# Optimization experiments

Hardware: AMD Instinct MI355X
Metric: run time of the kernel (lower is better)

Reference implementation:

```python
import jax, jax.numpy as jnp
import numpy as np

WIN = 11
SIGMA = 1.5
C1 = 0.01 ** 2
C2 = 0.03 ** 2


def _gauss1d():
    coords = jnp.arange(WIN, dtype=jnp.float32) - WIN // 2
    g = jnp.exp(-(coords ** 2) / (2.0 * SIGMA ** 2))
    return g / g.sum()


def _blur(x, g):
    C = x.shape[1]
    pad = WIN // 2
    dn = ('NCHW', 'OIHW', 'NCHW')
    kh = jnp.tile(g.reshape(1, 1, WIN, 1), (C, 1, 1, 1))
    kw = jnp.tile(g.reshape(1, 1, 1, WIN), (C, 1, 1, 1))
    x = jax.lax.conv_general_dilated(x, kh, (1, 1), ((pad, pad), (0, 0)),
                                     dimension_numbers=dn, feature_group_count=C)
    x = jax.lax.conv_general_dilated(x, kw, (1, 1), ((0, 0), (pad, pad)),
                                     dimension_numbers=dn, feature_group_count=C)
    return x


def _ssim_loss(pred, target, loss_weight=1.0):
    g = _gauss1d()
    mu1 = _blur(pred, g)
    mu2 = _blur(target, g)
    mu1_sq = mu1 * mu1
    mu2_sq = mu2 * mu2
    mu1_mu2 = mu1 * mu2
    sigma1_sq = _blur(pred * pred, g) - mu1_sq
    sigma2_sq = _blur(target * target, g) - mu2_sq
    sigma12 = _blur(pred * target, g) - mu1_mu2
    ssim_map = ((2.0 * mu1_mu2 + C1) * (2.0 * sigma12 + C2)) / \
               ((mu1_sq + mu2_sq + C1) * (sigma1_sq + sigma2_sq + C2))
    # size_average=True -> scalar mean; reduction='mean' on a scalar is identity
    return loss_weight * (1.0 - ssim_map.mean())


def setup_inputs() -> dict:
    key = jax.random.key(0)
    k1, k2 = jax.random.split(key)
    shape = (16, 3, 512, 512)
    pred = jax.random.uniform(k1, shape, dtype=jnp.float32)
    target = jax.random.uniform(k2, shape, dtype=jnp.float32)
    return {"pred": pred, "target": target}


def reference(pred, target):
    return _ssim_loss(pred, target, loss_weight=1.0)
```

## Files before the change

### kernel.cpp

```cpp
#include <hip/hip_runtime.h>

typedef float f2 __attribute__((ext_vector_type(2)));

#define IMG 512
#define TW 32
#define TH 32
#define NG 12
#define SROW 148
#define BOFFD 96
#define N_TOT (16 * 3 * 512 * 512)
#define NBLK (256 * 48)
#define NSLOT 1024

__device__ __constant__ f2 Gw2[11] = {
    {0.00102838f, 0.00102838f}, {0.00759876f, 0.00759876f},
    {0.03600077f, 0.03600077f}, {0.10936086f, 0.10936086f},
    {0.21300537f, 0.21300537f}, {0.26601173f, 0.26601173f},
    {0.21300537f, 0.21300537f}, {0.10936086f, 0.10936086f},
    {0.03600077f, 0.03600077f}, {0.00759876f, 0.00759876f},
    {0.00102838f, 0.00102838f}};

__device__ __forceinline__ unsigned pkh(float a, float b) {
    unsigned r;
    asm("v_cvt_pkrtz_f16_f32 %0, %1, %2" : "=v"(r) : "v"(a), "v"(b));
    return r;
}
__device__ __forceinline__ f2 uph(unsigned u) {
    float lo, hi;
    const unsigned uh = u >> 16;
    asm("v_cvt_f32_f16 %0, %1" : "=v"(lo) : "v"(u));
    asm("v_cvt_f32_f16 %0, %1" : "=v"(hi) : "v"(uh));
    return (f2){lo, hi};
}

__device__ __forceinline__ void vtaps(const float4 P, const float4 T, const int k,
                                      f2 A0[4][2], f2 A1[4][2]) {
    const f2 p[2] = {{P.x, P.y}, {P.z, P.w}};
    const f2 t[2] = {{T.x, T.y}, {T.z, T.w}};
#pragma unroll
    for (int h = 0; h < 2; ++h) {
        const f2 ss = p[h] * p[h] + t[h] * t[h];
        const f2 pt = p[h] * t[h];
        if (k < 11) {
            const f2 w = Gw2[k];
            A0[0][h] += w * p[h];
            A0[1][h] += w * t[h];
            A0[2][h] += w * ss;
            A0[3][h] += w * pt;
        }
        if (k > 0) {
            const f2 w = Gw2[k - 1];
            A1[0][h] += w * p[h];
            A1[1][h] += w * t[h];
            A1[2][h] += w * ss;
            A1[3][h] += w * pt;
        }
    }
}

__global__ __launch_bounds__(256, 4) void ssim_main(const float* __restrict__ pred,
                                                    const float* __restrict__ tgt,
                                                    float* __restrict__ ws,
                                                    int parts_mode) {
    __shared__ __align__(16) float plane[TH * SROW];
    __shared__ float red[4];

    const int tid = threadIdx.x;
    const int tile = blockIdx.x;
    const int plane_id = blockIdx.y;
    const int tile_x = tile & 15;
    const int tile_y = tile >> 4;
    const int tx = tile_x * TW;
    const int ty = tile_y * TH;
    const float* pbase = pred + (size_t)plane_id * (IMG * IMG);
    const float* tbase = tgt + (size_t)plane_id * (IMG * IMG);

    if (tid < NG * 16) {
        const int g4 = tid % NG;
        const int rp = tid / NG;
        const int r0 = rp * 2;
        const int col = tx - 8 + (g4 << 2);
        const int ybase = ty + r0 - 5;

        f2 A0[4][2], A1[4][2];
#pragma unroll
        for (int q = 0; q < 4; ++q)
#pragma unroll
            for (int h = 0; h < 2; ++h) { A0[q][h] = (f2)0.f; A1[q][h] = (f2)0.f; }

        if ((unsigned)(tile_x - 1) < 14u && (unsigned)(tile_y - 1) < 14u) {
            const float* pp = pbase + (ybase * IMG + col);
            const float* tp = tbase + (ybase * IMG + col);
#pragma unroll
            for (int k = 0; k < 12; ++k) {
                const float4 P = *(const float4*)(pp + k * IMG);
                const float4 T = *(const float4*)(tp + k * IMG);
                vtaps(P, T, k, A0, A1);
            }
        } else {
            const bool xin = (unsigned)col < (unsigned)IMG;
#pragma unroll
            for (int k = 0; k < 12; ++k) {
                const int y = ybase + k;
                float4 P = make_float4(0.f, 0.f, 0.f, 0.f);
                float4 T = make_float4(0.f, 0.f, 0.f, 0.f);
                if (xin && (unsigned)y < (unsigned)IMG) {
                    const int gidx = y * IMG + col;
                    P = *(const float4*)(pbase + gidx);
                    T = *(const float4*)(tbase + gidx);
                }
                vtaps(P, T, k, A0, A1);
            }
        }

        const int cb = g4 << 2;
#pragma unroll
        for (int r = 0; r < 2; ++r) {
            f2 (*A)[2] = r ? A1 : A0;
            float* rowA = &plane[(r0 + r) * SROW + (cb << 1)];
            *(float4*)rowA       = make_float4(A[0][0].x, A[1][0].x, A[0][0].y, A[1][0].y);
            *(float4*)(rowA + 4) = make_float4(A[0][1].x, A[1][1].x, A[0][1].y, A[1][1].y);
            uint4 bv;
            bv.x = pkh(A[2][0].x, A[3][0].x);
            bv.y = pkh(A[2][0].y, A[3][0].y);
            bv.z = pkh(A[2][1].x, A[3][1].x);
            bv.w = pkh(A[2][1].y, A[3][1].y);
            *(uint4*)&plane[(r0 + r) * SROW + BOFFD + cb] = bv;
        }
    }
    __syncthreads();

    float lsum = 0.f;
    {
        const int oy = tid >> 3;
        const int ox = (tid & 7) << 2;
        const float* rowbase = &plane[oy * SROW];

        f2 acc[4];
        f2 sacc[4];
#pragma unroll
        for (int j = 0; j < 4; ++j) { acc[j] = (f2)0.f; sacc[j] = (f2)0.f; }

        {
            const float4* rowA = (const float4*)(rowbase + ((ox + 2) << 1));
#pragma unroll
            for (int i4 = 0; i4 < 8; ++i4) {
                const float4 q = rowA[i4];
                const f2 v[2] = {{q.x, q.y}, {q.z, q.w}};
#pragma unroll
                for (int h = 0; h < 2; ++h) {
                    const int i = 2 * i4 + h;
#pragma unroll
                    for (int j = 0; j < 4; ++j) {
                        const int k = i - 1 - j;
                        if (k >= 0 && k <= 10) acc[j] += Gw2[k] * v[h];
                    }
                }
            }
        }

        {
            const uint4* rowB = (const uint4*)(rowbase + BOFFD + ox);
#pragma unroll
            for (int i4 = 0; i4 < 5; ++i4) {
                const uint4 q = rowB[i4];
                const unsigned qq[4] = {q.x, q.y, q.z, q.w};
#pragma unroll
                for (int c = 0; c < 4; ++c) {
                    const int m = 4 * i4 + c;
                    if (m >= 3 && m <= 16) {
                        const f2 v = uph(qq[c]);
#pragma unroll
                        for (int j = 0; j < 4; ++j) {
                            const int k = m - 3 - j;
                            if (k >= 0 && k <= 10) sacc[j] += Gw2[k] * v;
                        }
                    }
                }
            }
        }

        const float C1 = 0.0001f;
        const float C2 = 0.0009f;
#pragma unroll
        for (int j = 0; j < 4; ++j) {
            const float m1 = acc[j].x, m2 = acc[j].y;
            const float bss = sacc[j].x, bpt = sacc[j].y;
            const float mu1s = m1 * m1;
            const float mu2s = m2 * m2;
            const float mu12 = m1 * m2;
            const float A = mu1s + mu2s;
            const float s12 = bpt - mu12;
            const float sden = bss - A;
            const float num = fmaf(2.f, mu12, C1) * fmaf(2.f, s12, C2);
            const float den = (A + C1) * (sden + C2);
            lsum += num * __builtin_amdgcn_rcpf(den);
        }
    }

#pragma unroll
    for (int off = 32; off > 0; off >>= 1) lsum += __shfl_down(lsum, off, 64);
    if ((tid & 63) == 0) red[tid >> 6] = lsum;
    __syncthreads();
    if (tid == 0) {
        const float bs = (red[0] + red[1]) + (red[2] + red[3]);
        const int bid = blockIdx.y * gridDim.x + blockIdx.x;
        if (parts_mode) {
            ws[bid] = bs;
        } else {
            atomicAdd(&ws[bid & (NSLOT - 1)], bs);
        }
    }
}

__global__ __launch_bounds__(1024) void ssim_final(const float4* __restrict__ ws4,
                                                   float* __restrict__ out, int count4) {
    __shared__ float red[16];
    const int tid = threadIdx.x;
    float s = 0.f;
    for (int i = tid; i < count4; i += 1024) {
        const float4 w = ws4[i];
        s += (w.x + w.y) + (w.z + w.w);
    }
#pragma unroll
    for (int off = 32; off > 0; off >>= 1) s += __shfl_down(s, off, 64);
    if ((tid & 63) == 0) red[tid >> 6] = s;
    __syncthreads();
    if (tid == 0) {
        float tot = 0.f;
#pragma unroll
        for (int i = 0; i < 16; ++i) tot += red[i];
        out[0] = 1.0f - tot * (1.0f / (float)N_TOT);
    }
}

extern "C" void kernel_launch(void* const* d_in, const int* in_sizes, int n_in,
                              void* d_out, int out_size, void* d_ws, size_t ws_size,
                              hipStream_t stream) {
    const float* pred = (const float*)d_in[0];
    const float* tgt = (const float*)d_in[1];
    float* out = (float*)d_out;
    float* ws = (float*)d_ws;

    const int parts_mode = (ws_size >= (size_t)NBLK * sizeof(float)) ? 1 : 0;
    if (!parts_mode) {
        hipMemsetAsync(ws, 0, NSLOT * sizeof(float), stream);
    }
    dim3 grid(256, 48);
    ssim_main<<<grid, 256, 0, stream>>>(pred, tgt, ws, parts_mode);
    ssim_final<<<1, 1024, 0, stream>>>((const float4*)ws, out,
                                       (parts_mode ? NBLK : NSLOT) / 4);
}
```

Measured before the change: 166.4 us.

## Convert to persistent blocks with per-XCD atomic work queues over tiles

Replaces the 256x48 one-tile-per-block grid with 1024 persistent blocks. Each block pulls tile tasks from a per-XCD atomic counter, so every XCD works on a fixed set of 32 spatial tiles across all planes, meant to improve L2 locality for halo rows. The next task index is fetched before the barrier to hide the atomic latency. Per-block launch overhead and the large partial-sum array go away, at the cost of atomic contention, an extra barrier per task, and correctness relying on blockIdx.x&7 matching the hardware XCD assignment.

```diff
diff --git a/kernel.cpp b/kernel.cpp
--- a/kernel.cpp
+++ b/kernel.cpp
@@ -9,8 +9,11 @@
 #define SROW 148
 #define BOFFD 96
 #define N_TOT (16 * 3 * 512 * 512)
-#define NBLK (256 * 48)
-#define NSLOT 1024
+#define NPLANES 48
+#define NTASK (NPLANES * 32)
+#define GRID_X 1024
+#define CNT_STRIDE 32
+#define PART_OFF 512
 
 __device__ __constant__ f2 Gw2[11] = {
     {0.00102838f, 0.00102838f}, {0.00759876f, 0.00759876f},
@@ -60,142 +63,156 @@
 
 __global__ __launch_bounds__(256, 4) void ssim_main(const float* __restrict__ pred,
                                                     const float* __restrict__ tgt,
-                                                    float* __restrict__ ws,
-                                                    int parts_mode) {
+                                                    float* __restrict__ ws) {
     __shared__ __align__(16) float plane[TH * SROW];
     __shared__ float red[4];
+    __shared__ int sh_task[2];
 
     const int tid = threadIdx.x;
-    const int tile = blockIdx.x;
-    const int plane_id = blockIdx.y;
-    const int tile_x = tile & 15;
-    const int tile_y = tile >> 4;
-    const int tx = tile_x * TW;
-    const int ty = tile_y * TH;
-    const float* pbase = pred + (size_t)plane_id * (IMG * IMG);
-    const float* tbase = tgt + (size_t)plane_id * (IMG * IMG);
-
-    if (tid < NG * 16) {
-        const int g4 = tid % NG;
-        const int rp = tid / NG;
-        const int r0 = rp * 2;
-        const int col = tx - 8 + (g4 << 2);
-        const int ybase = ty + r0 - 5;
-
-        f2 A0[4][2], A1[4][2];
-#pragma unroll
-        for (int q = 0; q < 4; ++q)
-#pragma unroll
-            for (int h = 0; h < 2; ++h) { A0[q][h] = (f2)0.f; A1[q][h] = (f2)0.f; }
-
-        if ((unsigned)(tile_x - 1) < 14u && (unsigned)(tile_y - 1) < 14u) {
-            const float* pp = pbase + (ybase * IMG + col);
-            const float* tp = tbase + (ybase * IMG + col);
-#pragma unroll
-            for (int k = 0; k < 12; ++k) {
-                const float4 P = *(const float4*)(pp + k * IMG);
-                const float4 T = *(const float4*)(tp + k * IMG);
-                vtaps(P, T, k, A0, A1);
-            }
-        } else {
-            const bool xin = (unsigned)col < (unsigned)IMG;
-#pragma unroll
-            for (int k = 0; k < 12; ++k) {
-                const int y = ybase + k;
-                float4 P = make_float4(0.f, 0.f, 0.f, 0.f);
-                float4 T = make_float4(0.f, 0.f, 0.f, 0.f);
-                if (xin && (unsigned)y < (unsigned)IMG) {
-                    const int gidx = y * IMG + col;
-                    P = *(const float4*)(pbase + gidx);
-                    T = *(const float4*)(tbase + gidx);
-                }
-                vtaps(P, T, k, A0, A1);
-            }
-        }
-
-        const int cb = g4 << 2;
-#pragma unroll
-        for (int r = 0; r < 2; ++r) {
-            f2 (*A)[2] = r ? A1 : A0;
-            float* rowA = &plane[(r0 + r) * SROW + (cb << 1)];
-            *(float4*)rowA       = make_float4(A[0][0].x, A[1][0].x, A[0][0].y, A[1][0].y);
-            *(float4*)(rowA + 4) = make_float4(A[0][1].x, A[1][1].x, A[0][1].y, A[1][1].y);
-            uint4 bv;
-            bv.x = pkh(A[2][0].x, A[3][0].x);
-            bv.y = pkh(A[2][0].y, A[3][0].y);
-            bv.z = pkh(A[2][1].x, A[3][1].x);
-            bv.w = pkh(A[2][1].y, A[3][1].y);
-            *(uint4*)&plane[(r0 + r) * SROW + BOFFD + cb] = bv;
-        }
-    }
+    const int xcd = blockIdx.x & 7;
+    unsigned* cnt = (unsigned*)ws + (size_t)xcd * CNT_STRIDE;
+
+    if (tid == 0) sh_task[0] = (int)atomicAdd(cnt, 1u);
     __syncthreads();
 
     float lsum = 0.f;
-    {
-        const int oy = tid >> 3;
-        const int ox = (tid & 7) << 2;
-        const float* rowbase = &plane[oy * SROW];
-
-        f2 acc[4];
-        f2 sacc[4];
-#pragma unroll
-        for (int j = 0; j < 4; ++j) { acc[j] = (f2)0.f; sacc[j] = (f2)0.f; }
+    for (int it = 0;; ++it) {
+        const int t = __builtin_amdgcn_readfirstlane(sh_task[it & 1]);
+        if (t >= NTASK) break;
+        const int plane_id = t >> 5;
+        const int chunk = t & 31;
+        const int tile = (xcd << 5) | chunk;
+        const int tile_x = tile & 15;
+        const int tile_y = tile >> 4;
+        const int tx = tile_x * TW;
+        const int ty = tile_y * TH;
+        const float* pbase = pred + (size_t)plane_id * (IMG * IMG);
+        const float* tbase = tgt + (size_t)plane_id * (IMG * IMG);
+
+        if (tid < NG * 16) {
+            const int g4 = tid % NG;
+            const int rp = tid / NG;
+            const int r0 = rp * 2;
+            const int col = tx - 8 + (g4 << 2);
+            const int ybase = ty + r0 - 5;
+
+            f2 A0[4][2], A1[4][2];
+#pragma unroll
+            for (int q = 0; q < 4; ++q)
+#pragma unroll
+                for (int h = 0; h < 2; ++h) { A0[q][h] = (f2)0.f; A1[q][h] = (f2)0.f; }
+
+            if ((unsigned)(tile_x - 1) < 14u && (unsigned)(tile_y - 1) < 14u) {
+                const float* pp = pbase + (ybase * IMG + col);
+                const float* tp = tbase + (ybase * IMG + col);
+#pragma unroll
+                for (int k = 0; k < 12; ++k) {
+                    const float4 P = *(const float4*)(pp + k * IMG);
+                    const float4 T = *(const float4*)(tp + k * IMG);
+                    vtaps(P, T, k, A0, A1);
+                }
+            } else {
+                const bool xin = (unsigned)col < (unsigned)IMG;
+#pragma unroll
+                for (int k = 0; k < 12; ++k) {
+                    const int y = ybase + k;
+                    float4 P = make_float4(0.f, 0.f, 0.f, 0.f);
+                    float4 T = make_float4(0.f, 0.f, 0.f, 0.f);
+                    if (xin && (unsigned)y < (unsigned)IMG) {
+                        const int gidx = y * IMG + col;
+                        P = *(const float4*)(pbase + gidx);
+                        T = *(const float4*)(tbase + gidx);
+                    }
+                    vtaps(P, T, k, A0, A1);
+                }
+            }
+
+            const int cb = g4 << 2;
+#pragma unroll
+            for (int r = 0; r < 2; ++r) {
+                f2 (*A)[2] = r ? A1 : A0;
+                float* rowA = &plane[(r0 + r) * SROW + (cb << 1)];
+                *(float4*)rowA       = make_float4(A[0][0].x, A[1][0].x, A[0][0].y, A[1][0].y);
+                *(float4*)(rowA + 4) = make_float4(A[0][1].x, A[1][1].x, A[0][1].y, A[1][1].y);
+                uint4 bv;
+                bv.x = pkh(A[2][0].x, A[3][0].x);
+                bv.y = pkh(A[2][0].y, A[3][0].y);
+                bv.z = pkh(A[2][1].x, A[3][1].x);
+                bv.w = pkh(A[2][1].y, A[3][1].y);
+                *(uint4*)&plane[(r0 + r) * SROW + BOFFD + cb] = bv;
+            }
+        }
+
+        if (tid == 0) sh_task[(it + 1) & 1] = (int)atomicAdd(cnt, 1u);
+        __syncthreads();
 
         {
-            const float4* rowA = (const float4*)(rowbase + ((ox + 2) << 1));
-#pragma unroll
-            for (int i4 = 0; i4 < 8; ++i4) {
-                const float4 q = rowA[i4];
-                const f2 v[2] = {{q.x, q.y}, {q.z, q.w}};
-#pragma unroll
-                for (int h = 0; h < 2; ++h) {
-                    const int i = 2 * i4 + h;
-#pragma unroll
-                    for (int j = 0; j < 4; ++j) {
-                        const int k = i - 1 - j;
-                        if (k >= 0 && k <= 10) acc[j] += Gw2[k] * v[h];
-                    }
-                }
-            }
-        }
-
-        {
-            const uint4* rowB = (const uint4*)(rowbase + BOFFD + ox);
-#pragma unroll
-            for (int i4 = 0; i4 < 5; ++i4) {
-                const uint4 q = rowB[i4];
-                const unsigned qq[4] = {q.x, q.y, q.z, q.w};
-#pragma unroll
-                for (int c = 0; c < 4; ++c) {
-                    const int m = 4 * i4 + c;
-                    if (m >= 3 && m <= 16) {
-                        const f2 v = uph(qq[c]);
+            const int oy = tid >> 3;
+            const int ox = (tid & 7) << 2;
+            const float* rowbase = &plane[oy * SROW];
+
+            f2 acc[4];
+            f2 sacc[4];
+#pragma unroll
+            for (int j = 0; j < 4; ++j) { acc[j] = (f2)0.f; sacc[j] = (f2)0.f; }
+
+            {
+                const float4* rowA = (const float4*)(rowbase + ((ox + 2) << 1));
+#pragma unroll
+                for (int i4 = 0; i4 < 8; ++i4) {
+                    const float4 q = rowA[i4];
+                    const f2 v[2] = {{q.x, q.y}, {q.z, q.w}};
+#pragma unroll
+                    for (int h = 0; h < 2; ++h) {
+                        const int i = 2 * i4 + h;
 #pragma unroll
                         for (int j = 0; j < 4; ++j) {
-                            const int k = m - 3 - j;
-                            if (k >= 0 && k <= 10) sacc[j] += Gw2[k] * v;
+                            const int k = i - 1 - j;
+                            if (k >= 0 && k <= 10) acc[j] += Gw2[k] * v[h];
                         }
                     }
                 }
             }
-        }
-
-        const float C1 = 0.0001f;
-        const float C2 = 0.0009f;
-#pragma unroll
-        for (int j = 0; j < 4; ++j) {
-            const float m1 = acc[j].x, m2 = acc[j].y;
-            const float bss = sacc[j].x, bpt = sacc[j].y;
-            const float mu1s = m1 * m1;
-            const float mu2s = m2 * m2;
-            const float mu12 = m1 * m2;
-            const float A = mu1s + mu2s;
-            const float s12 = bpt - mu12;
-            const float sden = bss - A;
-            const float num = fmaf(2.f, mu12, C1) * fmaf(2.f, s12, C2);
-            const float den = (A + C1) * (sden + C2);
-            lsum += num * __builtin_amdgcn_rcpf(den);
-        }
+
+            {
+                const uint4* rowB = (const uint4*)(rowbase + BOFFD + ox);
+#pragma unroll
+                for (int i4 = 0; i4 < 5; ++i4) {
+                    const uint4 q = rowB[i4];
+                    const unsigned qq[4] = {q.x, q.y, q.z, q.w};
+#pragma unroll
+                    for (int c = 0; c < 4; ++c) {
+                        const int m = 4 * i4 + c;
+                        if (m >= 3 && m <= 16) {
+                            const f2 v = uph(qq[c]);
+#pragma unroll
+                            for (int j = 0; j < 4; ++j) {
+                                const int k = m - 3 - j;
+                                if (k >= 0 && k <= 10) sacc[j] += Gw2[k] * v;
+                            }
+                        }
+                    }
+                }
+            }
+
+            const float C1 = 0.0001f;
+            const float C2 = 0.0009f;
+#pragma unroll
+            for (int j = 0; j < 4; ++j) {
+                const float m1 = acc[j].x, m2 = acc[j].y;
+                const float bss = sacc[j].x, bpt = sacc[j].y;
+                const float mu1s = m1 * m1;
+                const float mu2s = m2 * m2;
+                const float mu12 = m1 * m2;
+                const float A = mu1s + mu2s;
+                const float s12 = bpt - mu12;
+                const float sden = bss - A;
+                const float num = fmaf(2.f, mu12, C1) * fmaf(2.f, s12, C2);
+                const float den = (A + C1) * (sden + C2);
+                lsum += num * __builtin_amdgcn_rcpf(den);
+            }
+        }
+        __syncthreads();
     }
 
 #pragma unroll
@@ -203,13 +220,7 @@
     if ((tid & 63) == 0) red[tid >> 6] = lsum;
     __syncthreads();
     if (tid == 0) {
-        const float bs = (red[0] + red[1]) + (red[2] + red[3]);
-        const int bid = blockIdx.y * gridDim.x + blockIdx.x;
-        if (parts_mode) {
-            ws[bid] = bs;
-        } else {
-            atomicAdd(&ws[bid & (NSLOT - 1)], bs);
-        }
+        ws[PART_OFF + blockIdx.x] = (red[0] + red[1]) + (red[2] + red[3]);
     }
 }
 
@@ -242,12 +253,7 @@
     float* out = (float*)d_out;
     float* ws = (float*)d_ws;
 
-    const int parts_mode = (ws_size >= (size_t)NBLK * sizeof(float)) ? 1 : 0;
-    if (!parts_mode) {
-        hipMemsetAsync(ws, 0, NSLOT * sizeof(float), stream);
-    }
-    dim3 grid(256, 48);
-    ssim_main<<<grid, 256, 0, stream>>>(pred, tgt, ws, parts_mode);
-    ssim_final<<<1, 1024, 0, stream>>>((const float4*)ws, out,
-                                       (parts_mode ? NBLK : NSLOT) / 4);
-}
+    hipMemsetAsync(ws, 0, 1024, stream);
+    ssim_main<<<dim3(GRID_X), 256, 0, stream>>>(pred, tgt, ws);
+    ssim_final<<<1, 1024, 0, stream>>>((const float4*)(ws + PART_OFF), out, GRID_X / 4);
+}
```

Measured after the change: 165.6 us. Within noise of the previous version (-0.5%).
